# Performance work log

Hardware: AMD Instinct MI355X
Metric: run time of the kernel (lower is better)

## Reference

```python
import jax, jax.numpy as jnp
import numpy as np

B, L, D, V = 512, 128, 512, 100000

def setup_inputs() -> dict:
    key = jax.random.key(0)
    ks = jax.random.split(key, 8)
    return {
        "t1s": jax.random.randint(ks[0], (B,), 0, V),
        "t2s": jax.random.randint(ks[1], (B,), 0, V),
        "t1_contexts": jax.random.randint(ks[2], (B, L), 0, V),
        "t2_contexts": jax.random.randint(ks[3], (B, L), 0, V),
        "embed_table": jax.random.normal(ks[4], (V, D), dtype=jnp.float32),
        "att_mat": jax.random.normal(ks[5], (D, D), dtype=jnp.float32) * (6.0 / (D + D)) ** 0.5,
        "w_pred": jax.random.normal(ks[6], (D, 1), dtype=jnp.float32) * 0.02,
        "b_pred": jnp.zeros((1,), dtype=jnp.float32),
    }

def _frob_normalize(x):
    # torch.norm(mat, p=2) is the Frobenius norm of the whole (L, D) matrix
    n = jnp.sqrt(jnp.sum(x * x, axis=(1, 2), keepdims=True))
    return x / n

def reference(t1s, t2s, t1_contexts, t2_contexts, embed_table, att_mat, w_pred, b_pred):
    # dropout is identity in eval mode; t1s/t2s embeddings are unused in the
    # 'dynamic' branch (dead code in the original forward).
    A = _frob_normalize(embed_table[t1_contexts])  # (B, L, D)
    Bm = _frob_normalize(embed_table[t2_contexts])  # (B, L, D)
    # batched bilinear attention: tanh(A @ att_mat @ B^T)
    S = jnp.tanh(jnp.einsum('bld,de,bme->blm', A, att_mat, Bm))  # (B, L, L)
    rows = jax.nn.softmax(jnp.mean(S, axis=2), axis=1)  # (B, L)
    cols = jax.nn.softmax(jnp.mean(S, axis=1), axis=1)  # (B, L)
    newA = jnp.einsum('bld,bl->bd', A, rows)   # (B, D)
    newB = jnp.einsum('bld,bl->bd', Bm, cols)  # (B, D)
    logits = ((newA * newB) @ w_pred + b_pred).reshape(-1)  # (B,)
    return logits, S
```

## Files before the change

### kernel.cpp

```cpp
#include <hip/hip_runtime.h>
#include <hip/hip_bf16.h>
#include <stdint.h>

#define NB 512
#define NL 128
#define ND 512

typedef __bf16 bf16;
typedef __bf16 bf16x8 __attribute__((ext_vector_type(8)));
typedef float  f32x4  __attribute__((ext_vector_type(4)));

#define GLDS(src, dst) __builtin_amdgcn_global_load_lds( \
    (const __attribute__((address_space(1))) void*)(src), \
    (__attribute__((address_space(3))) void*)(dst), 16, 0, 0)

__global__ __launch_bounds__(256) void k_attT(const float* __restrict__ att,
                                              bf16* __restrict__ attT) {
    int i = blockIdx.x * 256 + threadIdx.x;
    int n = i >> 9, k = i & 511;
    attT[i] = (bf16)att[k * 512 + n];
}

__global__ __launch_bounds__(512) void k_mega(
        const int* __restrict__ ctx1, const int* __restrict__ ctx2,
        const float* __restrict__ table, const bf16* __restrict__ attT,
        bf16* __restrict__ Ab, bf16* __restrict__ Bb,
        float* __restrict__ Sout, const float* __restrict__ w_pred,
        const float* __restrict__ b_pred, float* __restrict__ logits) {
    const int b = blockIdx.x, row0 = b * NL, tid = threadIdx.x;
    const int lane = tid & 63, w = tid >> 6;
    const int lm = lane & 15, quad = lane >> 4;
    const int wm  = (w & 1) * 64;
    const int wn1 = (w >> 1) * 128;
    const int wn2 = (w >> 1) * 32;

    __shared__ __align__(16) char smem[163840];
    bf16* stA0 = (bf16*)smem;
    bf16* stA1 = (bf16*)(smem + 8192);
    bf16* stT0 = (bf16*)(smem + 16384);
    bf16* stT1 = (bf16*)(smem + 49152);
    float* red = (float*)(smem + 81920);
    bf16* Tls  = (bf16*)smem;
    bf16* sB0  = (bf16*)(smem + 131072);
    bf16* sB1  = (bf16*)(smem + 139264);
    bf16* sC0  = (bf16*)(smem + 147456);
    bf16* sC1  = (bf16*)(smem + 155648);
    float* rowb = (float*)smem;
    float* colb = (float*)(smem + 2048);
    float* wrow = (float*)(smem + 3072);
    float* wcol = (float*)(smem + 3584);
    float* red2 = (float*)(smem + 4096);

    const int r8 = tid >> 6, c8 = tid & 63;
    float pa = 0.f, pb = 0.f;
    #pragma unroll 4
    for (int j = 0; j < 16; ++j) {
        int l = j * 8 + r8;
        int ia = ctx1[row0 + l], ib = ctx2[row0 + l];
        const float4* ra = (const float4*)table + (size_t)ia * (ND / 4) + c8 * 2;
        const float4* rb = (const float4*)table + (size_t)ib * (ND / 4) + c8 * 2;
        float4 a0 = ra[0], a1 = ra[1];
        float4 b0 = rb[0], b1 = rb[1];
        pa += a0.x*a0.x + a0.y*a0.y + a0.z*a0.z + a0.w*a0.w
            + a1.x*a1.x + a1.y*a1.y + a1.z*a1.z + a1.w*a1.w;
        pb += b0.x*b0.x + b0.y*b0.y + b0.z*b0.z + b0.w*b0.w
            + b1.x*b1.x + b1.y*b1.y + b1.z*b1.z + b1.w*b1.w;
        union { bf16 h[8]; uint4 u; } ua, ub;
        ua.h[0]=(bf16)a0.x; ua.h[1]=(bf16)a0.y; ua.h[2]=(bf16)a0.z; ua.h[3]=(bf16)a0.w;
        ua.h[4]=(bf16)a1.x; ua.h[5]=(bf16)a1.y; ua.h[6]=(bf16)a1.z; ua.h[7]=(bf16)a1.w;
        ub.h[0]=(bf16)b0.x; ub.h[1]=(bf16)b0.y; ub.h[2]=(bf16)b0.z; ub.h[3]=(bf16)b0.w;
        ub.h[4]=(bf16)b1.x; ub.h[5]=(bf16)b1.y; ub.h[6]=(bf16)b1.z; ub.h[7]=(bf16)b1.w;
        *(uint4*)(Ab + (size_t)(row0 + l) * ND + c8 * 8) = ua.u;
        *(uint4*)(Bb + (size_t)(row0 + l) * ND + c8 * 8) = ub.u;
    }
    for (int o = 32; o; o >>= 1) { pa += __shfl_xor(pa, o); pb += __shfl_xor(pb, o); }
    if (lane == 0) { red[w * 2] = pa; red[w * 2 + 1] = pb; }
    __syncthreads();
    float ssA = 0.f, ssB = 0.f;
    #pragma unroll
    for (int i = 0; i < 8; ++i) { ssA += red[i * 2]; ssB += red[i * 2 + 1]; }

    #define STAGE1(k0, dA, dT) do {                                          \
        { int r_ = tid >> 2, sl_ = tid & 3, cs_ = sl_ ^ ((r_ >> 1) & 3);     \
          GLDS(Ab + (size_t)(row0 + r_) * ND + (k0) + cs_ * 8, (dA) + tid * 8); } \
        _Pragma("unroll")                                                    \
        for (int i_ = 0; i_ < 4; ++i_) {                                     \
            int s_ = i_ * 512 + tid, r_ = s_ >> 2, sl_ = s_ & 3;             \
            int cs_ = sl_ ^ ((r_ >> 1) & 3);                                 \
            GLDS(attT + (size_t)r_ * ND + (k0) + cs_ * 8, (dT) + s_ * 8); }  \
    } while (0)
    #define STAGE2(k0, dB, dC) do {                                          \
        int r_ = tid >> 2, sl_ = tid & 3, cs_ = sl_ ^ ((r_ >> 1) & 3);       \
        GLDS(Bb + (size_t)(row0 + r_) * ND + (k0) + cs_ * 8, (dB) + tid * 8);\
        GLDS(Ab + (size_t)(row0 + r_) * ND + (k0) + cs_ * 8, (dC) + tid * 8);\
    } while (0)

    f32x4 acc1[4][8] = {};
    STAGE1(0, stA0, stT0);

    for (int t = 0; t < 16; ++t) {
        if (t < 15) {
            STAGE1((t + 1) * 32, (t & 1) ? stA0 : stA1, (t & 1) ? stT0 : stT1);
            asm volatile("s_waitcnt vmcnt(5)" ::: "memory");
        } else {
            STAGE2(0, sB0, sC0);
            asm volatile("s_waitcnt vmcnt(2)" ::: "memory");
        }
        __builtin_amdgcn_s_barrier();
        const bf16* A_ = (t & 1) ? stA1 : stA0;
        const bf16* T_ = (t & 1) ? stT1 : stT0;
        bf16x8 af[4], bfm[8];
        #pragma unroll
        for (int t4 = 0; t4 < 4; ++t4) {
            int R = wm + t4 * 16 + lm;
            af[t4] = *(const bf16x8*)&A_[R * 32 + (quad ^ ((R >> 1) & 3)) * 8];
        }
        #pragma unroll
        for (int t8 = 0; t8 < 8; ++t8) {
            int R = wn1 + t8 * 16 + lm;
            bfm[t8] = *(const bf16x8*)&T_[R * 32 + (quad ^ ((R >> 1) & 3)) * 8];
        }
        __builtin_amdgcn_s_setprio(1);
        #pragma unroll
        for (int im = 0; im < 4; ++im)
            #pragma unroll
            for (int jn = 0; jn < 8; ++jn)
                acc1[im][jn] = __builtin_amdgcn_mfma_f32_16x16x32_bf16(
                    af[im], bfm[jn], acc1[im][jn], 0, 0, 0);
        __builtin_amdgcn_s_setprio(0);
        __builtin_amdgcn_s_barrier();
    }

    #pragma unroll
    for (int im = 0; im < 4; ++im)
    #pragma unroll
    for (int jn = 0; jn < 8; ++jn)
    #pragma unroll
    for (int p = 0; p < 4; ++p) {
        int m = wm + im * 16 + quad * 4 + p;
        int n = wn1 + jn * 16 + lm;
        int ks = n >> 5, kq = (n >> 3) & 3, e = n & 7;
        int pos = kq ^ ((m >> 2) & 3);
        Tls[ks * 4096 + m * 32 + pos * 8 + e] = (bf16)acc1[im][jn][p];
    }
    __syncthreads();

    f32x4 acc2[4][2] = {}, accG[4][2] = {};

    for (int t = 0; t < 16; ++t) {
        if (t < 15) {
            STAGE2((t + 1) * 32, (t & 1) ? sB0 : sB1, (t & 1) ? sC0 : sC1);
            asm volatile("s_waitcnt vmcnt(2)" ::: "memory");
        } else {
            asm volatile("s_waitcnt vmcnt(0)" ::: "memory");
        }
        __builtin_amdgcn_s_barrier();
        const bf16* B_ = (t & 1) ? sB1 : sB0;
        const bf16* C_ = (t & 1) ? sC1 : sC0;
        float4 w0 = *(const float4*)(w_pred + t * 32 + quad * 8);
        float4 w1 = *(const float4*)(w_pred + t * 32 + quad * 8 + 4);
        float wv[8] = {w0.x, w0.y, w0.z, w0.w, w1.x, w1.y, w1.z, w1.w};
        bf16x8 af[4], af2[4], bf2[2], bfw[2];
        #pragma unroll
        for (int t4 = 0; t4 < 4; ++t4) {
            int R = wm + t4 * 16 + lm;
            af[t4]  = *(const bf16x8*)&Tls[t * 4096 + R * 32 + (quad ^ ((R >> 2) & 3)) * 8];
            af2[t4] = *(const bf16x8*)&C_[R * 32 + (quad ^ ((R >> 1) & 3)) * 8];
        }
        #pragma unroll
        for (int t2 = 0; t2 < 2; ++t2) {
            int R = wn2 + t2 * 16 + lm;
            bf2[t2] = *(const bf16x8*)&B_[R * 32 + (quad ^ ((R >> 1) & 3)) * 8];
            #pragma unroll
            for (int j = 0; j < 8; ++j)
                bfw[t2][j] = (bf16)((float)bf2[t2][j] * wv[j]);
        }
        __builtin_amdgcn_s_setprio(1);
        #pragma unroll
        for (int im = 0; im < 4; ++im)
            #pragma unroll
            for (int jn = 0; jn < 2; ++jn) {
                acc2[im][jn] = __builtin_amdgcn_mfma_f32_16x16x32_bf16(
                    af[im], bf2[jn], acc2[im][jn], 0, 0, 0);
                accG[im][jn] = __builtin_amdgcn_mfma_f32_16x16x32_bf16(
                    af2[im], bfw[jn], accG[im][jn], 0, 0, 0);
            }
        __builtin_amdgcn_s_setprio(0);
        __builtin_amdgcn_s_barrier();
    }

    const float sc = rsqrtf(ssA * ssB);
    float* __restrict__ Sb = Sout + (size_t)b * NL * NL;
    #pragma unroll
    for (int im = 0; im < 4; ++im)
    #pragma unroll
    for (int jn = 0; jn < 2; ++jn)
    #pragma unroll
    for (int p = 0; p < 4; ++p) {
        float v = tanhf(acc2[im][jn][p] * sc);
        acc2[im][jn][p] = v;
        int m = wm + im * 16 + quad * 4 + p;
        int n = wn2 + jn * 16 + lm;
        __builtin_nontemporal_store(v, &Sb[m * NL + n]);
    }
    #pragma unroll
    for (int im = 0; im < 4; ++im)
    #pragma unroll
    for (int p = 0; p < 4; ++p) {
        float r = acc2[im][0][p] + acc2[im][1][p];
        r += __shfl_xor(r, 1); r += __shfl_xor(r, 2);
        r += __shfl_xor(r, 4); r += __shfl_xor(r, 8);
        if (lm == 0) rowb[(w >> 1) * NL + wm + im * 16 + quad * 4 + p] = r;
    }
    #pragma unroll
    for (int jn = 0; jn < 2; ++jn) {
        float cv = 0.f;
        #pragma unroll
        for (int im = 0; im < 4; ++im)
            #pragma unroll
            for (int p = 0; p < 4; ++p) cv += acc2[im][jn][p];
        cv += __shfl_xor(cv, 16); cv += __shfl_xor(cv, 32);
        if (quad == 0) colb[(w & 1) * NL + wn2 + jn * 16 + lm] = cv;
    }
    __syncthreads();

    if (tid < 64) {
        float a  = (rowb[tid] + rowb[NL + tid] + rowb[2 * NL + tid] + rowb[3 * NL + tid]) * (1.f / NL);
        float c2 = (rowb[tid + 64] + rowb[NL + tid + 64] + rowb[2 * NL + tid + 64] + rowb[3 * NL + tid + 64]) * (1.f / NL);
        float mx = fmaxf(a, c2);
        for (int o = 32; o; o >>= 1) mx = fmaxf(mx, __shfl_xor(mx, o));
        float e0 = expf(a - mx), e1 = expf(c2 - mx);
        float s = e0 + e1;
        for (int o = 32; o; o >>= 1) s += __shfl_xor(s, o);
        float inv = 1.f / s;
        wrow[tid] = e0 * inv; wrow[tid + 64] = e1 * inv;
    } else if (tid < 128) {
        int q = tid - 64;
        float a  = (colb[q] + colb[NL + q]) * (1.f / NL);
        float c2 = (colb[q + 64] + colb[NL + q + 64]) * (1.f / NL);
        float mx = fmaxf(a, c2);
        for (int o = 32; o; o >>= 1) mx = fmaxf(mx, __shfl_xor(mx, o));
        float e0 = expf(a - mx), e1 = expf(c2 - mx);
        float s = e0 + e1;
        for (int o = 32; o; o >>= 1) s += __shfl_xor(s, o);
        float inv = 1.f / s;
        wcol[q] = e0 * inv; wcol[q + 64] = e1 * inv;
    }
    __syncthreads();

    float wc0 = wcol[wn2 + lm], wc1 = wcol[wn2 + 16 + lm];
    float g = 0.f;
    #pragma unroll
    for (int im = 0; im < 4; ++im)
    #pragma unroll
    for (int p = 0; p < 4; ++p) {
        float wr = wrow[wm + im * 16 + quad * 4 + p];
        g += wr * (wc0 * accG[im][0][p] + wc1 * accG[im][1][p]);
    }
    for (int o = 32; o; o >>= 1) g += __shfl_xor(g, o);
    if (lane == 0) red2[w] = g;
    __syncthreads();
    if (tid == 0) {
        float tot = 0.f;
        #pragma unroll
        for (int i = 0; i < 8; ++i) tot += red2[i];
        logits[b] = tot * sc + b_pred[0];
    }
}

extern "C" void kernel_launch(void* const* d_in, const int* in_sizes, int n_in,
                              void* d_out, int out_size, void* d_ws, size_t ws_size,
                              hipStream_t stream) {
    const int*   t1c = (const int*)d_in[2];
    const int*   t2c = (const int*)d_in[3];
    const float* emb = (const float*)d_in[4];
    const float* att = (const float*)d_in[5];
    const float* wp  = (const float*)d_in[6];
    const float* bp  = (const float*)d_in[7];

    float* out    = (float*)d_out;
    float* logits = out;
    float* S      = out + NB;

    char* ws = (char*)d_ws;
    bf16*  Ab   = (bf16*)(ws);
    bf16*  Bb   = (bf16*)(ws + 67108864);
    bf16*  attT = (bf16*)(ws + 134217728);

    k_attT<<<dim3(1024), 256, 0, stream>>>(att, attT);
    k_mega<<<dim3(NB), 512, 0, stream>>>(t1c, t2c, emb, attT, Ab, Bb,
                                         S, wp, bp, logits);
}
```

Baseline: 388.2 us.

## Split embedding gather and norm into a separate high-parallelism kernel

```diff
diff --git a/kernel.cpp b/kernel.cpp
--- a/kernel.cpp
+++ b/kernel.cpp
@@ -14,18 +14,54 @@
     (const __attribute__((address_space(1))) void*)(src), \
     (__attribute__((address_space(3))) void*)(dst), 16, 0, 0)
 
-__global__ __launch_bounds__(256) void k_attT(const float* __restrict__ att,
-                                              bf16* __restrict__ attT) {
-    int i = blockIdx.x * 256 + threadIdx.x;
-    int n = i >> 9, k = i & 511;
-    attT[i] = (bf16)att[k * 512 + n];
+__global__ __launch_bounds__(256) void k_gather(const int* __restrict__ ctx1,
+                                                const int* __restrict__ ctx2,
+                                                const float* __restrict__ table,
+                                                bf16* __restrict__ d1,
+                                                bf16* __restrict__ d2,
+                                                float* __restrict__ ss,
+                                                const float* __restrict__ att,
+                                                bf16* __restrict__ attT) {
+    const int b = blockIdx.x, side = blockIdx.y, zc = blockIdx.z, t = threadIdx.x;
+    if (side == 2) {
+        int chunk = b * 8 + zc;
+        if (chunk < 1024) {
+            int i = chunk * 256 + t;
+            int n = i >> 9, k = i & 511;
+            attT[i] = (bf16)att[k * 512 + n];
+        }
+        return;
+    }
+    const int* __restrict__ ctx = side ? ctx2 : ctx1;
+    bf16* __restrict__ dst = side ? d2 : d1;
+    const int base = b * NL;
+    const int dv = t & 127, lr = t >> 7;
+    int idxs[8];
+    #pragma unroll
+    for (int i = 0; i < 8; ++i) idxs[i] = ctx[base + zc * 16 + i * 2 + lr];
+    float acc = 0.f;
+    #pragma unroll
+    for (int i = 0; i < 8; ++i) {
+        int l = zc * 16 + i * 2 + lr;
+        f32x4 v = __builtin_nontemporal_load(
+            (const f32x4*)table + (size_t)idxs[i] * (ND / 4) + dv);
+        acc += v[0]*v[0] + v[1]*v[1] + v[2]*v[2] + v[3]*v[3];
+        union { bf16 h[4]; uint2 u; } pk;
+        pk.h[0] = (bf16)v[0]; pk.h[1] = (bf16)v[1];
+        pk.h[2] = (bf16)v[2]; pk.h[3] = (bf16)v[3];
+        *((uint2*)(dst + (size_t)(base + l) * ND) + dv) = pk.u;
+    }
+    for (int o = 32; o; o >>= 1) acc += __shfl_xor(acc, o);
+    __shared__ float red[4];
+    if ((t & 63) == 0) red[t >> 6] = acc;
+    __syncthreads();
+    if (t == 0) atomicAdd(&ss[side * NB + b], red[0] + red[1] + red[2] + red[3]);
 }
 
-__global__ __launch_bounds__(512) void k_mega(
-        const int* __restrict__ ctx1, const int* __restrict__ ctx2,
-        const float* __restrict__ table, const bf16* __restrict__ attT,
-        bf16* __restrict__ Ab, bf16* __restrict__ Bb,
-        float* __restrict__ Sout, const float* __restrict__ w_pred,
+__global__ __launch_bounds__(512) void k_mega2(
+        const bf16* __restrict__ Ab, const bf16* __restrict__ attT,
+        const bf16* __restrict__ Bb, float* __restrict__ Sout,
+        const float* __restrict__ ss, const float* __restrict__ w_pred,
         const float* __restrict__ b_pred, float* __restrict__ logits) {
     const int b = blockIdx.x, row0 = b * NL, tid = threadIdx.x;
     const int lane = tid & 63, w = tid >> 6;
@@ -39,7 +75,6 @@
     bf16* stA1 = (bf16*)(smem + 8192);
     bf16* stT0 = (bf16*)(smem + 16384);
     bf16* stT1 = (bf16*)(smem + 49152);
-    float* red = (float*)(smem + 81920);
     bf16* Tls  = (bf16*)smem;
     bf16* sB0  = (bf16*)(smem + 131072);
     bf16* sB1  = (bf16*)(smem + 139264);
@@ -51,34 +86,7 @@
     float* wcol = (float*)(smem + 3584);
     float* red2 = (float*)(smem + 4096);
 
-    const int r8 = tid >> 6, c8 = tid & 63;
-    float pa = 0.f, pb = 0.f;
-    #pragma unroll 4
-    for (int j = 0; j < 16; ++j) {
-        int l = j * 8 + r8;
-        int ia = ctx1[row0 + l], ib = ctx2[row0 + l];
-        const float4* ra = (const float4*)table + (size_t)ia * (ND / 4) + c8 * 2;
-        const float4* rb = (const float4*)table + (size_t)ib * (ND / 4) + c8 * 2;
-        float4 a0 = ra[0], a1 = ra[1];
-        float4 b0 = rb[0], b1 = rb[1];
-        pa += a0.x*a0.x + a0.y*a0.y + a0.z*a0.z + a0.w*a0.w
-            + a1.x*a1.x + a1.y*a1.y + a1.z*a1.z + a1.w*a1.w;
-        pb += b0.x*b0.x + b0.y*b0.y + b0.z*b0.z + b0.w*b0.w
-            + b1.x*b1.x + b1.y*b1.y + b1.z*b1.z + b1.w*b1.w;
-        union { bf16 h[8]; uint4 u; } ua, ub;
-        ua.h[0]=(bf16)a0.x; ua.h[1]=(bf16)a0.y; ua.h[2]=(bf16)a0.z; ua.h[3]=(bf16)a0.w;
-        ua.h[4]=(bf16)a1.x; ua.h[5]=(bf16)a1.y; ua.h[6]=(bf16)a1.z; ua.h[7]=(bf16)a1.w;
-        ub.h[0]=(bf16)b0.x; ub.h[1]=(bf16)b0.y; ub.h[2]=(bf16)b0.z; ub.h[3]=(bf16)b0.w;
-        ub.h[4]=(bf16)b1.x; ub.h[5]=(bf16)b1.y; ub.h[6]=(bf16)b1.z; ub.h[7]=(bf16)b1.w;
-        *(uint4*)(Ab + (size_t)(row0 + l) * ND + c8 * 8) = ua.u;
-        *(uint4*)(Bb + (size_t)(row0 + l) * ND + c8 * 8) = ub.u;
-    }
-    for (int o = 32; o; o >>= 1) { pa += __shfl_xor(pa, o); pb += __shfl_xor(pb, o); }
-    if (lane == 0) { red[w * 2] = pa; red[w * 2 + 1] = pb; }
-    __syncthreads();
-    float ssA = 0.f, ssB = 0.f;
-    #pragma unroll
-    for (int i = 0; i < 8; ++i) { ssA += red[i * 2]; ssB += red[i * 2 + 1]; }
+    const float ssA = ss[b], ssB = ss[NB + b];
 
     #define STAGE1(k0, dA, dT) do {                                          \
         { int r_ = tid >> 2, sl_ = tid & 3, cs_ = sl_ ^ ((r_ >> 1) & 3);     \
@@ -286,8 +294,9 @@
     bf16*  Ab   = (bf16*)(ws);
     bf16*  Bb   = (bf16*)(ws + 67108864);
     bf16*  attT = (bf16*)(ws + 134217728);
-
-    k_attT<<<dim3(1024), 256, 0, stream>>>(att, attT);
-    k_mega<<<dim3(NB), 512, 0, stream>>>(t1c, t2c, emb, attT, Ab, Bb,
-                                         S, wp, bp, logits);
+    float* ss   = (float*)(ws + 134742016);
+
+    hipMemsetAsync(ss, 0, 4096, stream);
+    k_gather<<<dim3(NB, 3, 8), 256, 0, stream>>>(t1c, t2c, emb, Ab, Bb, ss, att, attT);
+    k_mega2<<<dim3(NB), 512, 0, stream>>>(Ab, attT, Bb, S, ss, wp, bp, logits);
 }
```

Result: slower. 398.5 us (+2.7%).
